# Kernel tuning notes

Hardware: AMD Instinct MI355X
Metric: run time of the kernel (lower is better)

The kernel has to match this reference:

```python
import jax, jax.numpy as jnp
import numpy as np

# DPLayer config (init kwargs)
MAX_OP = False            # False -> min-plus (shortest path) semiring; null = +inf
MAKE_POS = True           # GraphLayer make_pos: force positive edge weights
NULL = -1e30 if MAX_OP else 1e30   # finite stand-in for +/-inf (grad-safe)
B, H, W = 512, 256, 256


def setup_inputs() -> dict:
    key = jax.random.key(0)
    images = jax.random.normal(key, (B, 1, H, W), dtype=jnp.float32)
    return {"images": images}


def _edge_weights(images):
    # GraphLayer: edge_f('euclidean') on pixel values, made positive via softplus.
    x = images[:, 0, :, :]                       # [B, H, W] node/edge costs theta
    if MAKE_POS:
        x = jax.nn.softplus(x)
    return x


def _dp(theta):
    # V[i,j] = theta[i,j] + comb(V[i-1,j], V[i-1,j-1], V[i,j-1]); comb = min (max_op=False)
    # Row recurrence is solved in parallel via prefix-sum + associative running-min:
    #   A[j] = comb(V[i-1,j], V[i-1,j-1])
    #   V[i,j] = S[j] + runmin_{k<=j}(A[k] - S[k-1]),  S = cumsum(theta row)
    comb = jnp.maximum if MAX_OP else jnp.minimum
    null = jnp.asarray(NULL, theta.dtype)
    b = theta.shape[0]

    v0 = jnp.cumsum(theta[:, 0, :], axis=-1)     # first row: only right moves

    def row_step(vprev, th_row):                 # vprev: [B,W], th_row: [B,W]
        shifted = jnp.concatenate([jnp.full((b, 1), null, theta.dtype), vprev[:, :-1]], axis=1)
        A = comb(vprev, shifted)                 # best of up / up-left
        S = jnp.cumsum(th_row, axis=-1)
        Sprev = jnp.concatenate([jnp.zeros((b, 1), theta.dtype), S[:, :-1]], axis=1)
        V = S + jax.lax.associative_scan(comb, A - Sprev, axis=-1)
        return V, None

    vlast, _ = jax.lax.scan(row_step, v0, jnp.moveaxis(theta[:, 1:, :], 1, 0))
    return vlast[:, -1]                          # path length to (H-1, W-1), [B]


def reference(images):
    theta = _edge_weights(images)
    fake_lengths = _dp(theta)
    return fake_lengths
```

## Files before the change

kernel.cpp:

```cpp
#include <hip/hip_runtime.h>


#define HH 256
#define WW 256
#define CH 16
#define NCH 16
#define NULLV 1e30f

template<int CTRL, int ROWM>
__device__ __forceinline__ float dpp_mov(float x, float oldv) {
    return __builtin_bit_cast(float, __builtin_amdgcn_update_dpp(
        __builtin_bit_cast(int, oldv), __builtin_bit_cast(int, x),
        CTRL, ROWM, 0xF, false));
}

__device__ __forceinline__ float wave_iscan_min(float x) {
    asm volatile(
        "s_nop 1\n\t"
        "v_min_f32_dpp %0, %0, %0 row_shr:1  row_mask:0xf bank_mask:0xf\n\t"
        "s_nop 1\n\t"
        "v_min_f32_dpp %0, %0, %0 row_shr:2  row_mask:0xf bank_mask:0xf\n\t"
        "s_nop 1\n\t"
        "v_min_f32_dpp %0, %0, %0 row_shr:4  row_mask:0xf bank_mask:0xf\n\t"
        "s_nop 1\n\t"
        "v_min_f32_dpp %0, %0, %0 row_shr:8  row_mask:0xf bank_mask:0xf\n\t"
        "s_nop 1\n\t"
        "v_min_f32_dpp %0, %0, %0 row_bcast:15 row_mask:0xa bank_mask:0xf\n\t"
        "s_nop 1\n\t"
        "v_min_f32_dpp %0, %0, %0 row_bcast:31 row_mask:0xc bank_mask:0xf"
        : "+v"(x));
    return x;
}

__device__ __forceinline__ float wave_iscan_add(float x) {
    asm volatile(
        "s_nop 1\n\t"
        "v_add_f32_dpp %0, %0, %0 row_shr:1  row_mask:0xf bank_mask:0xf bound_ctrl:0\n\t"
        "s_nop 1\n\t"
        "v_add_f32_dpp %0, %0, %0 row_shr:2  row_mask:0xf bank_mask:0xf bound_ctrl:0\n\t"
        "s_nop 1\n\t"
        "v_add_f32_dpp %0, %0, %0 row_shr:4  row_mask:0xf bank_mask:0xf bound_ctrl:0\n\t"
        "s_nop 1\n\t"
        "v_add_f32_dpp %0, %0, %0 row_shr:8  row_mask:0xf bank_mask:0xf bound_ctrl:0\n\t"
        "s_nop 1\n\t"
        "v_add_f32_dpp %0, %0, %0 row_bcast:15 row_mask:0xa bank_mask:0xf bound_ctrl:0\n\t"
        "s_nop 1\n\t"
        "v_add_f32_dpp %0, %0, %0 row_bcast:31 row_mask:0xc bank_mask:0xf bound_ctrl:0"
        : "+v"(x));
    return x;
}

__device__ __forceinline__ float softplus_f(float x) {
    float ax = fabsf(x);
    float t  = __expf(-ax);
    return fmaxf(x, 0.0f) + __logf(1.0f + t);
}

__device__ __forceinline__ float4 prep_row(float4 c) {
    float t0 = softplus_f(c.x);
    float t1 = t0 + softplus_f(c.y);
    float t2 = t1 + softplus_f(c.z);
    float t3 = t2 + softplus_f(c.w);
    float s    = wave_iscan_add(t3);
    float soff = dpp_mov<0x138, 0xF>(s, 0.0f);
    return make_float4(soff + t0, soff + t1, soff + t2, soff + t3);
}

template<int NR>
__device__ __forceinline__ void load_rows(const float4* gp, int r0, float4* L) {
#pragma unroll
    for (int i = 0; i < NR; ++i) L[i] = gp[(size_t)(r0 + i) * 64];
}

template<int NR>
__device__ __forceinline__ void prep_store(const float4* L, float* dst, int lane) {
#pragma unroll
    for (int i = 0; i < NR; ++i)
        *reinterpret_cast<float4*>(&dst[i * WW + lane * 4]) = prep_row(L[i]);
}

template<int NR>
__device__ __forceinline__ void prep_run(const float4* gp, int row0,
                                         float* base0, float* base1, int lane) {
    float4 L[NR];
    load_rows<NR>(gp, CH + row0, L);
    __syncthreads();
    for (int k = 1; k < NCH; ++k) {
        float4 N[NR];
        if (k + 1 < NCH) load_rows<NR>(gp, (k + 1) * CH + row0, N);
        prep_store<NR>(L, (k & 1) ? base1 : base0, lane);
        __syncthreads();
        if (k + 1 < NCH) {
#pragma unroll
            for (int i = 0; i < NR; ++i) L[i] = N[i];
        }
    }
}

__global__ __launch_bounds__(448, 2) void dp_kernel(const float* __restrict__ img,
                                                    float* __restrict__ out) {
    const int tid = threadIdx.x;
    const int wid = tid >> 6;
    const int lane = tid & 63;

    __shared__ __align__(16) float sbuf[2][CH][WW];

    const float* gbase = img + (size_t)blockIdx.x * HH * WW;
    const float4* gp = reinterpret_cast<const float4*>(gbase) + lane;

    if (wid == 3) {
        {
            float4 C[2];
            load_rows<2>(gp, 0, C);
            prep_store<2>(C, &sbuf[0][0][0], lane);
        }
        __syncthreads();
        __builtin_amdgcn_s_setprio(1);

        float v0, v1, v2, v3;
        auto row_step = [&](const float4& S) {
            float soff = dpp_mov<0x138, 0xF>(S.w, 0.0f);
            float vm1  = dpp_mov<0x138, 0xF>(v3, NULLV);
            float B0 = fminf(v0, vm1) - soff;
            float B1 = fminf(v1, v0) - S.x;
            float B2 = fminf(v2, v1) - S.y;
            float B3 = fminf(v3, v2) - S.z;
            float m1 = fminf(B0, B1);
            float p  = fminf(B2, B3);
            float m2 = fminf(m1, B2);
            float m3 = fminf(m1, p);
            float mm   = wave_iscan_min(m3);
            float moff = dpp_mov<0x138, 0xF>(mm, NULLV);
            v0 = S.x + fminf(moff, B0);
            v1 = S.y + fminf(moff, m1);
            v2 = S.z + fminf(moff, m2);
            v3 = S.w + fminf(moff, m3);
        };

#define RD8(P, buf, r0)                                                  \
    P##0 = *reinterpret_cast<const float4*>(&(buf)[(r0) + 0][lane * 4]); \
    P##1 = *reinterpret_cast<const float4*>(&(buf)[(r0) + 1][lane * 4]); \
    P##2 = *reinterpret_cast<const float4*>(&(buf)[(r0) + 2][lane * 4]); \
    P##3 = *reinterpret_cast<const float4*>(&(buf)[(r0) + 3][lane * 4]); \
    P##4 = *reinterpret_cast<const float4*>(&(buf)[(r0) + 4][lane * 4]); \
    P##5 = *reinterpret_cast<const float4*>(&(buf)[(r0) + 5][lane * 4]); \
    P##6 = *reinterpret_cast<const float4*>(&(buf)[(r0) + 6][lane * 4]); \
    P##7 = *reinterpret_cast<const float4*>(&(buf)[(r0) + 7][lane * 4]);
#define ST8(P)                                                           \
    row_step(P##0); row_step(P##1); row_step(P##2); row_step(P##3);      \
    row_step(P##4); row_step(P##5); row_step(P##6); row_step(P##7);

        float4 A0, A1, A2, A3, A4, A5, A6, A7;
        float4 B0, B1, B2, B3, B4, B5, B6, B7;

        {
            const float(*buf)[WW] = sbuf[0];
            RD8(A, buf, 0); RD8(B, buf, 8);
            v0 = A0.x; v1 = A0.y; v2 = A0.z; v3 = A0.w;
            row_step(A1); row_step(A2); row_step(A3);
            row_step(A4); row_step(A5); row_step(A6); row_step(A7);
            ST8(B);
        }
        for (int k = 1; k < NCH; ++k) {
            __syncthreads();
            const float(*buf)[WW] = sbuf[k & 1];
            RD8(A, buf, 0); RD8(B, buf, 8);
            ST8(A);
            ST8(B);
        }
#undef RD8
#undef ST8
        if (lane == 63) out[blockIdx.x] = v3;
    } else {
        if (wid == 0) { float4 C[3]; load_rows<3>(gp,  2, C); prep_store<3>(C, &sbuf[0][ 2][0], lane); }
        else if (wid == 1) { float4 C[3]; load_rows<3>(gp,  5, C); prep_store<3>(C, &sbuf[0][ 5][0], lane); }
        else if (wid == 2) { float4 C[3]; load_rows<3>(gp,  8, C); prep_store<3>(C, &sbuf[0][ 8][0], lane); }
        else if (wid == 4) { float4 C[2]; load_rows<2>(gp, 11, C); prep_store<2>(C, &sbuf[0][11][0], lane); }
        else if (wid == 5) { float4 C[2]; load_rows<2>(gp, 13, C); prep_store<2>(C, &sbuf[0][13][0], lane); }
        else               { float4 C[1]; load_rows<1>(gp, 15, C); prep_store<1>(C, &sbuf[0][15][0], lane); }

        if (wid == 0)      prep_run<3>(gp,  0, &sbuf[0][ 0][0], &sbuf[1][ 0][0], lane);
        else if (wid == 1) prep_run<3>(gp,  3, &sbuf[0][ 3][0], &sbuf[1][ 3][0], lane);
        else if (wid == 2) prep_run<3>(gp,  6, &sbuf[0][ 6][0], &sbuf[1][ 6][0], lane);
        else if (wid == 4) prep_run<3>(gp,  9, &sbuf[0][ 9][0], &sbuf[1][ 9][0], lane);
        else if (wid == 5) prep_run<2>(gp, 12, &sbuf[0][12][0], &sbuf[1][12][0], lane);
        else               prep_run<2>(gp, 14, &sbuf[0][14][0], &sbuf[1][14][0], lane);
    }
}

extern "C" void kernel_launch(void* const* d_in, const int* in_sizes, int n_in,
                              void* d_out, int out_size, void* d_ws, size_t ws_size,
                              hipStream_t stream) {
    const float* img = (const float*)d_in[0];
    float* out = (float*)d_out;
    dp_kernel<<<out_size, 448, 0, stream>>>(img, out);
}
```

Before: 38.43 us.

## Restructure DP row recurrence to defer wave scan and shorten critical path

Reformulates the per-row min-plus update so the state is kept as offsets m relative to the prefix sums S, and the wave-wide min scan result of the previous row is applied lazily via moff. Work that does not depend on the scan result (e.g. d/f terms from S alone) can then overlap with the serial DPP scan chain, shortening the loop-carried dependency per row. LDS reads are also reduced from 8-row to 4-row batches interleaved with compute, lowering register pressure. The cost is more VALU ops per row and a more intricate algebraic form that must match the reference exactly.

```diff
diff --git a/kernel.cpp b/kernel.cpp
--- a/kernel.cpp
+++ b/kernel.cpp
@@ -117,60 +117,71 @@
         __syncthreads();
         __builtin_amdgcn_s_setprio(1);
 
-        float v0, v1, v2, v3;
-        auto row_step = [&](const float4& S) {
-            float soff = dpp_mov<0x138, 0xF>(S.w, 0.0f);
-            float vm1  = dpp_mov<0x138, 0xF>(v3, NULLV);
-            float B0 = fminf(v0, vm1) - soff;
-            float B1 = fminf(v1, v0) - S.x;
-            float B2 = fminf(v2, v1) - S.y;
-            float B3 = fminf(v3, v2) - S.z;
-            float m1 = fminf(B0, B1);
-            float p  = fminf(B2, B3);
-            float m2 = fminf(m1, B2);
-            float m3 = fminf(m1, p);
-            float mm   = wave_iscan_min(m3);
+        float4 Sp;
+        float m0, m1, m2, m3;
+        float mm;
+        float soffp;
+
+        auto init_row0 = [&](const float4& S) {
+            Sp = S; m0 = m1 = m2 = m3 = 0.0f; mm = 0.0f;
+            soffp = dpp_mov<0x138, 0xF>(S.w, 0.0f);
+        };
+
+        auto row_step = [&](const float4& Sc) {
+            float u0 = Sp.x + m0, u1 = Sp.y + m1, u2 = Sp.z + m2, u3 = Sp.w + m3;
+            float c1 = fminf(u1, u0), c2 = fminf(u2, u1), c3 = fminf(u3, u2);
+            float d0 = fminf(Sp.x, soffp);
+            float d1 = fminf(Sp.y, Sp.x), d2 = fminf(Sp.z, Sp.y), d3 = fminf(Sp.w, Sp.z);
+            float soffc = dpp_mov<0x138, 0xF>(Sc.w, 0.0f);
+            float e0 = u0 - soffc, e1 = c1 - Sc.x, e2 = c2 - Sc.y, e3 = c3 - Sc.z;
+            float f0 = d0 - soffc, f1 = d1 - Sc.x, f2 = d2 - Sc.y, f3 = d3 - Sc.z;
+            float C1 = fminf(e0, e1), C2 = fminf(C1, e2);
+            float C3 = fminf(C1, fminf(e2, e3));
+            float D1 = fminf(f0, f1), D2 = fminf(D1, f2);
+            float D3 = fminf(D1, fminf(f2, f3));
             float moff = dpp_mov<0x138, 0xF>(mm, NULLV);
-            v0 = S.x + fminf(moff, B0);
-            v1 = S.y + fminf(moff, m1);
-            v2 = S.z + fminf(moff, m2);
-            v3 = S.w + fminf(moff, m3);
+            m0 = fminf(e0, moff + f0);
+            m1 = fminf(C1, moff + D1);
+            m2 = fminf(C2, moff + D2);
+            m3 = fminf(C3, moff + D3);
+            mm = wave_iscan_min(m3);
+            Sp = Sc; soffp = soffc;
         };
 
-#define RD8(P, buf, r0)                                                  \
+#define RD4(P, buf, r0)                                                  \
     P##0 = *reinterpret_cast<const float4*>(&(buf)[(r0) + 0][lane * 4]); \
     P##1 = *reinterpret_cast<const float4*>(&(buf)[(r0) + 1][lane * 4]); \
     P##2 = *reinterpret_cast<const float4*>(&(buf)[(r0) + 2][lane * 4]); \
-    P##3 = *reinterpret_cast<const float4*>(&(buf)[(r0) + 3][lane * 4]); \
-    P##4 = *reinterpret_cast<const float4*>(&(buf)[(r0) + 4][lane * 4]); \
-    P##5 = *reinterpret_cast<const float4*>(&(buf)[(r0) + 5][lane * 4]); \
-    P##6 = *reinterpret_cast<const float4*>(&(buf)[(r0) + 6][lane * 4]); \
-    P##7 = *reinterpret_cast<const float4*>(&(buf)[(r0) + 7][lane * 4]);
-#define ST8(P)                                                           \
-    row_step(P##0); row_step(P##1); row_step(P##2); row_step(P##3);      \
-    row_step(P##4); row_step(P##5); row_step(P##6); row_step(P##7);
-
-        float4 A0, A1, A2, A3, A4, A5, A6, A7;
-        float4 B0, B1, B2, B3, B4, B5, B6, B7;
+    P##3 = *reinterpret_cast<const float4*>(&(buf)[(r0) + 3][lane * 4]);
+#define ST4(P) row_step(P##0); row_step(P##1); row_step(P##2); row_step(P##3);
+
+        float4 A0, A1, A2, A3, B0, B1, B2, B3;
 
         {
             const float(*buf)[WW] = sbuf[0];
-            RD8(A, buf, 0); RD8(B, buf, 8);
-            v0 = A0.x; v1 = A0.y; v2 = A0.z; v3 = A0.w;
+            RD4(A, buf, 0); RD4(B, buf, 4);
+            init_row0(A0);
             row_step(A1); row_step(A2); row_step(A3);
-            row_step(A4); row_step(A5); row_step(A6); row_step(A7);
-            ST8(B);
+            RD4(A, buf, 8);
+            ST4(B);
+            RD4(B, buf, 12);
+            ST4(A);
+            ST4(B);
         }
         for (int k = 1; k < NCH; ++k) {
             __syncthreads();
             const float(*buf)[WW] = sbuf[k & 1];
-            RD8(A, buf, 0); RD8(B, buf, 8);
-            ST8(A);
-            ST8(B);
-        }
-#undef RD8
-#undef ST8
-        if (lane == 63) out[blockIdx.x] = v3;
+            RD4(A, buf, 0); RD4(B, buf, 4);
+            ST4(A);
+            RD4(A, buf, 8);
+            ST4(B);
+            RD4(B, buf, 12);
+            ST4(A);
+            ST4(B);
+        }
+#undef RD4
+#undef ST4
+        if (lane == 63) out[blockIdx.x] = Sp.w + mm;
     } else {
         if (wid == 0) { float4 C[3]; load_rows<3>(gp,  2, C); prep_store<3>(C, &sbuf[0][ 2][0], lane); }
         else if (wid == 1) { float4 C[3]; load_rows<3>(gp,  5, C); prep_store<3>(C, &sbuf[0][ 5][0], lane); }
```

Measured after the change: 43.41 us. +13.0%, slower.
